# Kernel optimization log

Hardware: AMD Instinct MI355X
Metric: run time of the kernel (lower is better)

The kernel has to match this reference:

```python
import jax, jax.numpy as jnp
import numpy as np

B, S, D, U, L, DEG = 32, 256, 256, 256, 16, 16
N = B * S
E = N * DEG


def _xavier(k, shape, fan_in, fan_out):
    return jax.random.normal(k, shape, jnp.float32) * np.float32(np.sqrt(2.0 / (fan_in + fan_out)))


def setup_inputs() -> dict:
    key = jax.random.key(0)
    ks = jax.random.split(key, 16)
    src = jax.random.normal(ks[0], (S, B, D), jnp.float32)
    V_in = _xavier(ks[1], (L, D, U), D, U)
    b_in = jnp.zeros((L, U), jnp.float32)
    V_in_gate = _xavier(ks[2], (D, 1), D, 1)
    b_in_gate = jnp.ones((L, 1), jnp.float32)
    V_out = _xavier(ks[3], (L, D, U), D, U)
    b_out = jnp.zeros((L, U), jnp.float32)
    V_out_gate = _xavier(ks[4], (D, 1), D, 1)
    b_out_gate = jnp.ones((L, 1), jnp.float32)
    W_self_loop = _xavier(ks[5], (D, U), D, U)
    W_self_loop_gate = _xavier(ks[6], (D, 1), D, 1)
    arc_tensor_in = jnp.stack([jax.random.randint(ks[7], (E,), 0, B),
                               jax.random.randint(ks[8], (E,), 0, S)]).astype(jnp.int64)
    arc_tensor_out = jnp.stack([jax.random.randint(ks[9], (E,), 0, B),
                                jax.random.randint(ks[10], (E,), 0, S)]).astype(jnp.int64)
    label_tensor_in = jax.random.randint(ks[11], (1, E), 0, L).astype(jnp.int64)
    label_tensor_out = jax.random.randint(ks[12], (1, E), 0, L).astype(jnp.int64)
    mask_in = jnp.ones((N, DEG), jnp.float32)
    mask_out = jnp.ones((N, DEG), jnp.float32)
    mask_loop = jnp.ones((N, 1), jnp.float32)
    sent_mask = jnp.ones((S, B), jnp.float32)
    return {"src": src, "V_in": V_in, "b_in": b_in, "V_in_gate": V_in_gate,
            "b_in_gate": b_in_gate, "V_out": V_out, "b_out": b_out,
            "V_out_gate": V_out_gate, "b_out_gate": b_out_gate,
            "W_self_loop": W_self_loop, "W_self_loop_gate": W_self_loop_gate,
            "arc_tensor_in": arc_tensor_in, "arc_tensor_out": arc_tensor_out,
            "label_tensor_in": label_tensor_in, "label_tensor_out": label_tensor_out,
            "mask_in": mask_in, "mask_out": mask_out, "mask_loop": mask_loop,
            "sent_mask": sent_mask}


def _gcn_forward(src, V_in, b_in, V_in_gate, b_in_gate, V_out, b_out, V_out_gate,
                 b_out_gate, W_self_loop, W_self_loop_gate, mask_in, mask_out,
                 mask_loop, sent_mask, arc_tensor_in, arc_tensor_out,
                 label_tensor_in, label_tensor_out):
    S_, B_, D_ = src.shape
    U_ = V_in.shape[-1]
    enc = jnp.transpose(src, (1, 0, 2))            # [B,S,D]
    x = enc.reshape(B_ * S_, D_)                   # [N,D]

    def arc_branch(V, b, Vg, bg, arc, lab):
        # per-label transform of all nodes, as in the original: [L,N,U]
        all_lab = jnp.einsum('nd,ldu->lnu', x, V)
        idx = arc[0] * S_ + arc[1]                 # [E] flat node indices
        l = lab[0]                                  # [E] edge labels
        feats = all_lab[l, idx] + b[l]              # [E,U]
        deg = idx.shape[0] // (B_ * S_)
        feats = feats.reshape(B_, S_, deg, U_)
        g = (x @ Vg)[idx, 0] + bg[l, 0]             # [E]
        gate = g.reshape(B_, S_, deg)
        return feats, gate

    in_, in_gate = arc_branch(V_in, b_in, V_in_gate, b_in_gate, arc_tensor_in, label_tensor_in)
    out_, out_gate = arc_branch(V_out, b_out, V_out_gate, b_out_gate, arc_tensor_out, label_tensor_out)
    same = (x @ W_self_loop).reshape(B_, S_, 1, U_)
    same_gate = (x @ W_self_loop_gate).reshape(B_, S_, 1)

    pot = jnp.concatenate([in_, out_, same], axis=2)            # [B,S,maxdeg,U]
    pot_gate = jnp.concatenate([in_gate, out_gate, same_gate], axis=2)
    mask_soft = jnp.concatenate([mask_in, mask_out, mask_loop], axis=1)  # [N,maxdeg]
    md = pot.shape[2]
    pot = pot.reshape(B_ * S_, md, U_)
    probs = jax.nn.sigmoid(pot_gate.reshape(B_ * S_, md)) * mask_soft
    res = jax.nn.relu(jnp.sum(pot * probs[:, :, None], axis=1)).reshape(B_, S_, U_)
    res = res * sent_mask.T[:, :, None]
    return jnp.transpose(res, (1, 0, 2))            # [S,B,U]


def reference(src, V_in, b_in, V_in_gate, b_in_gate, V_out, b_out, V_out_gate,
              b_out_gate, W_self_loop, W_self_loop_gate, arc_tensor_in,
              arc_tensor_out, label_tensor_in, label_tensor_out, mask_in,
              mask_out, mask_loop, sent_mask):
    return _gcn_forward(src, V_in, b_in, V_in_gate, b_in_gate, V_out, b_out,
                        V_out_gate, b_out_gate, W_self_loop, W_self_loop_gate,
                        mask_in, mask_out, mask_loop, sent_mask,
                        arc_tensor_in, arc_tensor_out, label_tensor_in,
                        label_tensor_out)
```

## Files before the change

### kernel.cpp

```cpp
#include <hip/hip_runtime.h>
#include <hip/hip_bf16.h>

#define BB 32
#define SS 256
#define DD 256
#define UU 256
#define LL 16
#define DEG 16
#define NN (BB * SS)
#define EE (NN * DEG)
#define NSLICE 33
#define NSL2 34
#define KMAIN (NSLICE * DD)
#define KTOT (NSL2 * DD)
#define KSPLIT 8
#define KS (KTOT / KSPLIT)
#define TM 128
#define TN 256

using short8 = __attribute__((ext_vector_type(8))) short;
using f32x4  = __attribute__((ext_vector_type(4))) float;

#define GLDS(g, l)                                                        \
  __builtin_amdgcn_global_load_lds(                                       \
      (const __attribute__((address_space(1))) void*)(g),                 \
      (__attribute__((address_space(3))) void*)(l), 16, 0, 0)

__device__ __forceinline__ float bf2f(unsigned short v) {
  union { unsigned u; float f; } t;
  t.u = ((unsigned)v) << 16;
  return t.f;
}
__device__ __forceinline__ unsigned short f2bf(float f) {
  __hip_bfloat16 h = __float2bfloat16(f);
  return *(unsigned short*)&h;
}
__device__ __forceinline__ float sigm(float x) {
  return 1.f / (1.f + __expf(-x));
}

__global__ __launch_bounds__(256) void k_pre(
    const float* __restrict__ src, const float* __restrict__ gin,
    const float* __restrict__ gout, const float* __restrict__ gloop,
    const float* __restrict__ Vin, const float* __restrict__ Vout,
    const float* __restrict__ Wself, const float* __restrict__ b_in,
    const float* __restrict__ b_out,
    __hip_bfloat16* __restrict__ x_bf, float* __restrict__ xg_in,
    float* __restrict__ xg_out, float* __restrict__ xg_loop,
    __hip_bfloat16* __restrict__ Vt) {
  int bid = blockIdx.x;
  if (bid < NN) {
    int n = bid;
    int b = n / SS, s = n % SS;
    int d = threadIdx.x;
    float v = src[(size_t)(s * BB + b) * DD + d];
    x_bf[(size_t)n * DD + d] = __float2bfloat16(v);
    float p0 = v * gin[d], p1 = v * gout[d], p2 = v * gloop[d];
#pragma unroll
    for (int o = 32; o > 0; o >>= 1) {
      p0 += __shfl_down(p0, o);
      p1 += __shfl_down(p1, o);
      p2 += __shfl_down(p2, o);
    }
    __shared__ float r0[4], r1[4], r2[4];
    int w = threadIdx.x >> 6, lane = threadIdx.x & 63;
    if (lane == 0) { r0[w] = p0; r1[w] = p1; r2[w] = p2; }
    __syncthreads();
    if (threadIdx.x == 0) {
      xg_in[n]   = r0[0] + r0[1] + r0[2] + r0[3];
      xg_out[n]  = r1[0] + r1[1] + r1[2] + r1[3];
      xg_loop[n] = r2[0] + r2[1] + r2[2] + r2[3];
    }
    return;
  }
  int t = bid - NN;
  int z = t >> 6;
  int rem = t & 63;
  int bx = rem & 7, by = rem >> 3;
  int tid = threadIdx.x;
  int tx = tid & 31, ty = tid >> 5;
  if (z == NSLICE) {
    int u0 = bx * 32, j0 = by * 32;
#pragma unroll
    for (int i = 0; i < 4; i++) {
      int u = u0 + ty + i * 8, j = j0 + tx;
      float v = 0.f;
      if (j >= 1 && j <= LL)         v = b_in[(j - 1) * UU + u];
      else if (j > LL && j < NSLICE) v = b_out[(j - 1 - LL) * UU + u];
      Vt[(size_t)u * KTOT + KMAIN + j] = __float2bfloat16(v);
    }
    return;
  }
  __shared__ float tbuf[32][33];
  const float* srcM = (z == 0) ? Wself
                    : (z <= LL ? Vin  + (size_t)(z - 1)      * DD * UU
                               : Vout + (size_t)(z - 1 - LL) * DD * UU);
  int u0 = bx * 32, d0 = by * 32;
#pragma unroll
  for (int i = 0; i < 4; i++) {
    int dr = ty + i * 8;
    tbuf[dr][tx] = srcM[(size_t)(d0 + dr) * UU + u0 + tx];
  }
  __syncthreads();
#pragma unroll
  for (int i = 0; i < 4; i++) {
    int ur = ty + i * 8;
    Vt[(size_t)(u0 + ur) * KTOT + z * DD + d0 + tx] = __float2bfloat16(tbuf[tx][ur]);
  }
}

__global__ __launch_bounds__(256) void k_agg(
    const __hip_bfloat16* __restrict__ x,
    const float* __restrict__ xg_in, const float* __restrict__ xg_out,
    const float* __restrict__ xg_loop,
    const float* __restrict__ b_ing, const float* __restrict__ b_outg,
    const int* __restrict__ arc_in, const int* __restrict__ arc_out,
    const int* __restrict__ lab_in, const int* __restrict__ lab_out,
    const float* __restrict__ mask_in, const float* __restrict__ mask_out,
    const float* __restrict__ mask_loop,
    __hip_bfloat16* __restrict__ Y) {
  __shared__ int u_sl[4][32], u_src[4][32];
  __shared__ float u_w[4][32];
  __shared__ int s_sl[4][32], s_src[4][32];
  __shared__ float s_w[4][32];
  __shared__ float s_wsum[4][NSLICE];
  int wv = threadIdx.x >> 6, lane = threadIdx.x & 63;
  int n = blockIdx.x * 4 + wv;
  if (lane < 32) {
    int br = lane >> 4, k = lane & 15;
    int e = n * DEG + k;
    const int* a = br ? arc_out : arc_in;
    int l = (br ? lab_out : lab_in)[e];
    int srcn = a[e] * SS + a[EE + e];
    float g = (br ? xg_out : xg_in)[srcn] + (br ? b_outg : b_ing)[l];
    u_sl[wv][lane] = 1 + br * LL + l;
    u_src[wv][lane] = srcn;
    u_w[wv][lane] = sigm(g) * (br ? mask_out : mask_in)[e];
  }
  __syncthreads();
  if (lane < 32) {
    int my = u_sl[wv][lane];
    int rank = 0;
#pragma unroll
    for (int j = 0; j < 32; j++) {
      int oj = u_sl[wv][j];
      rank += (oj < my || (oj == my && j < lane)) ? 1 : 0;
    }
    s_sl[wv][rank] = my;
    s_src[wv][rank] = u_src[wv][lane];
    s_w[wv][rank] = u_w[wv][lane];
  }
  __syncthreads();

  const unsigned short* xp = (const unsigned short*)x;
  unsigned short* yp = (unsigned short*)Y;
  int d4 = lane * 4;
  {
    float wl = sigm(xg_loop[n]) * mask_loop[n];
    ushort4 v = *(const ushort4*)&xp[(size_t)n * DD + d4];
    ushort4 o;
    o.x = f2bf(wl * bf2f(v.x)); o.y = f2bf(wl * bf2f(v.y));
    o.z = f2bf(wl * bf2f(v.z)); o.w = f2bf(wl * bf2f(v.w));
    *(ushort4*)&yp[(size_t)n * DD + d4] = o;
  }
  unsigned long long present = 0ull;
  float a0 = 0.f, a1 = 0.f, a2 = 0.f, a3 = 0.f, ws = 0.f;
#pragma unroll
  for (int e = 0; e < 32; e++) {
    int sl = s_sl[wv][e];
    int srcn = s_src[wv][e];
    float w = s_w[wv][e];
    ushort4 v = *(const ushort4*)&xp[(size_t)srcn * DD + d4];
    a0 += w * bf2f(v.x); a1 += w * bf2f(v.y);
    a2 += w * bf2f(v.z); a3 += w * bf2f(v.w);
    ws += w;
    int slnext = (e < 31) ? s_sl[wv][e + 1] : 999;
    if (sl != slnext) {
      ushort4 o;
      o.x = f2bf(a0); o.y = f2bf(a1); o.z = f2bf(a2); o.w = f2bf(a3);
      *(ushort4*)&yp[((size_t)sl * NN + n) * DD + d4] = o;
      if (lane == 0) s_wsum[wv][sl] = ws;
      present |= (1ull << sl);
      a0 = a1 = a2 = a3 = ws = 0.f;
    }
  }
  ushort4 zero4 = {0, 0, 0, 0};
#pragma unroll
  for (int s = 1; s < NSLICE; s++) {
    if (!((present >> s) & 1ull)) {
      *(ushort4*)&yp[((size_t)s * NN + n) * DD + d4] = zero4;
      if (lane == 0) s_wsum[wv][s] = 0.f;
    }
  }
  __syncthreads();
  {
    ushort4 o;
    unsigned short* op = (unsigned short*)&o;
#pragma unroll
    for (int c = 0; c < 4; c++) {
      int j = d4 + c;
      float v = (j >= 1 && j < NSLICE) ? s_wsum[wv][j] : 0.f;
      op[c] = f2bf(v);
    }
    *(ushort4*)&yp[((size_t)NSLICE * NN + n) * DD + d4] = o;
  }
}

__global__ __launch_bounds__(256, 2) void k_gemm(
    const __hip_bfloat16* __restrict__ A, const __hip_bfloat16* __restrict__ Bt,
    __hip_bfloat16* __restrict__ partial) {
  __shared__ __align__(16) __hip_bfloat16 As[2][TM * 32];
  __shared__ __align__(16) __hip_bfloat16 Bs[2][TN * 32];
  __hip_bfloat16* P = partial + (size_t)blockIdx.y * NN * UU;
  int kbeg = blockIdx.y * KS;
  int row0 = blockIdx.x * TM;
  int tid = threadIdx.x;
  int w = tid >> 6, lane = tid & 63;
  int lrow = lane & 15, quad = lane >> 4;
  int sr = lane >> 2;
  int sc = (lane & 3) * 8;

#define STAGE(bufi, it)                                                     \
  {                                                                         \
    int k0 = kbeg + (it) * 32;                                              \
    int sl = k0 >> 8, dc = k0 & 255;                                        \
    const __hip_bfloat16* Ab = A + ((size_t)sl * NN + row0) * DD + dc;      \
    _Pragma("unroll")                                                       \
    for (int t = 0; t < 2; t++) {                                           \
      int rb = (w * 2 + t) * 16;                                            \
      GLDS(&Ab[(size_t)(rb + sr) * DD + sc], &As[bufi][rb * 32]);           \
    }                                                                       \
    _Pragma("unroll")                                                       \
    for (int t = 0; t < 4; t++) {                                           \
      int rb = (w * 4 + t) * 16;                                            \
      GLDS(&Bt[(size_t)(rb + sr) * KTOT + k0 + sc], &Bs[bufi][rb * 32]);    \
    }                                                                       \
  }

  STAGE(0, 0);
  f32x4 acc[8][4] = {};
  constexpr int NIT = KS / 32;
  for (int it = 0; it < NIT; it++) {
    int cur = it & 1;
    __syncthreads();
    if (it + 1 < NIT) STAGE(cur ^ 1, it + 1);
    short8 af[8], bfr[4];
#pragma unroll
    for (int i = 0; i < 8; i++)
      af[i] = *(const short8*)&As[cur][(i * 16 + lrow) * 32 + quad * 8];
#pragma unroll
    for (int j = 0; j < 4; j++)
      bfr[j] = *(const short8*)&Bs[cur][(w * 64 + j * 16 + lrow) * 32 + quad * 8];
#pragma unroll
    for (int j = 0; j < 4; j++)
#pragma unroll
      for (int i = 0; i < 8; i++)
        acc[i][j] = __builtin_amdgcn_mfma_f32_16x16x32_bf16(af[i], bfr[j], acc[i][j], 0, 0, 0);
  }
#undef STAGE
#pragma unroll
  for (int i = 0; i < 8; i++)
#pragma unroll
    for (int j = 0; j < 4; j++) {
      int col = w * 64 + j * 16 + lrow;
      int rowb = row0 + i * 16 + quad * 4;
#pragma unroll
      for (int r = 0; r < 4; r++)
        P[(size_t)(rowb + r) * UU + col] = __float2bfloat16(acc[i][j][r]);
    }
}

__global__ __launch_bounds__(256) void k_finish(
    const __hip_bfloat16* __restrict__ partial, const float* __restrict__ sent,
    float* __restrict__ out) {
  int wv = threadIdx.x >> 6, lane = threadIdx.x & 63;
  int n = blockIdx.x * 4 + wv;
  int u4 = lane * 4;
  size_t idx = (size_t)n * UU + u4;
  const unsigned short* pp = (const unsigned short*)partial;
  float a0 = 0.f, a1 = 0.f, a2 = 0.f, a3 = 0.f;
#pragma unroll
  for (int z = 0; z < KSPLIT; z++) {
    ushort4 v = *(const ushort4*)&pp[(size_t)z * NN * UU + idx];
    a0 += bf2f(v.x); a1 += bf2f(v.y); a2 += bf2f(v.z); a3 += bf2f(v.w);
  }
  int s = n % SS, b = n / SS;
  float sm = sent[s * BB + b];
  float4 o;
  o.x = fmaxf(a0, 0.f) * sm; o.y = fmaxf(a1, 0.f) * sm;
  o.z = fmaxf(a2, 0.f) * sm; o.w = fmaxf(a3, 0.f) * sm;
  *(float4*)&out[((size_t)s * BB + b) * UU + u4] = o;
}

extern "C" void kernel_launch(void* const* d_in, const int* in_sizes, int n_in,
                              void* d_out, int out_size, void* d_ws, size_t ws_size,
                              hipStream_t stream) {
  const float* src      = (const float*)d_in[0];
  const float* V_in     = (const float*)d_in[1];
  const float* b_in     = (const float*)d_in[2];
  const float* V_ing    = (const float*)d_in[3];
  const float* b_ing    = (const float*)d_in[4];
  const float* V_out    = (const float*)d_in[5];
  const float* b_out    = (const float*)d_in[6];
  const float* V_outg   = (const float*)d_in[7];
  const float* b_outg   = (const float*)d_in[8];
  const float* W_self   = (const float*)d_in[9];
  const float* W_selfg  = (const float*)d_in[10];
  const int* arc_in     = (const int*)d_in[11];
  const int* arc_out    = (const int*)d_in[12];
  const int* lab_in     = (const int*)d_in[13];
  const int* lab_out    = (const int*)d_in[14];
  const float* mask_in  = (const float*)d_in[15];
  const float* mask_out = (const float*)d_in[16];
  const float* mask_loop= (const float*)d_in[17];
  const float* sent     = (const float*)d_in[18];
  float* out = (float*)d_out;

  char* ws = (char*)d_ws;
  size_t off = 0;
  auto alloc = [&](size_t bytes) -> void* {
    void* p = ws + off;
    off += (bytes + 255) & ~(size_t)255;
    return p;
  };
  __hip_bfloat16* x_bf = (__hip_bfloat16*)alloc((size_t)NN * DD * 2);
  __hip_bfloat16* Vt   = (__hip_bfloat16*)alloc((size_t)UU * KTOT * 2);
  float* xg_in   = (float*)alloc(NN * 4);
  float* xg_out  = (float*)alloc(NN * 4);
  float* xg_loop = (float*)alloc(NN * 4);
  __hip_bfloat16* Y = (__hip_bfloat16*)alloc((size_t)NSL2 * NN * DD * 2);
  __hip_bfloat16* partial =
      (__hip_bfloat16*)alloc((size_t)KSPLIT * NN * UU * 2);

  k_pre<<<NN + (NSLICE + 1) * 64, 256, 0, stream>>>(
      src, V_ing, V_outg, W_selfg, V_in, V_out, W_self, b_in, b_out,
      x_bf, xg_in, xg_out, xg_loop, Vt);
  k_agg<<<NN / 4, 256, 0, stream>>>(x_bf, xg_in, xg_out, xg_loop, b_ing, b_outg,
                                    arc_in, arc_out, lab_in, lab_out,
                                    mask_in, mask_out, mask_loop, Y);
  k_gemm<<<dim3(NN / TM, KSPLIT), 256, 0, stream>>>(Y, Vt, partial);
  k_finish<<<NN / 4, 256, 0, stream>>>(partial, sent, out);
}
```

Before: 194.4 us.

## Fuse preprocessing into aggregation and swizzle GEMM LDS layout

```diff
diff --git a/kernel.cpp b/kernel.cpp
--- a/kernel.cpp
+++ b/kernel.cpp
@@ -17,6 +17,8 @@
 #define KS (KTOT / KSPLIT)
 #define TM 128
 #define TN 256
+#define NAGG (NN / 4)
+#define NWT ((NSLICE + 1) * 64)
 
 using short8 = __attribute__((ext_vector_type(8))) short;
 using f32x4  = __attribute__((ext_vector_type(4))) float;
@@ -39,41 +41,120 @@
   return 1.f / (1.f + __expf(-x));
 }
 
-__global__ __launch_bounds__(256) void k_pre(
+__global__ __launch_bounds__(256) void k_front(
     const float* __restrict__ src, const float* __restrict__ gin,
     const float* __restrict__ gout, const float* __restrict__ gloop,
     const float* __restrict__ Vin, const float* __restrict__ Vout,
     const float* __restrict__ Wself, const float* __restrict__ b_in,
-    const float* __restrict__ b_out,
-    __hip_bfloat16* __restrict__ x_bf, float* __restrict__ xg_in,
-    float* __restrict__ xg_out, float* __restrict__ xg_loop,
-    __hip_bfloat16* __restrict__ Vt) {
+    const float* __restrict__ b_out, const float* __restrict__ b_ing,
+    const float* __restrict__ b_outg,
+    const int* __restrict__ arc_in, const int* __restrict__ arc_out,
+    const int* __restrict__ lab_in, const int* __restrict__ lab_out,
+    const float* __restrict__ mask_in, const float* __restrict__ mask_out,
+    const float* __restrict__ mask_loop,
+    __hip_bfloat16* __restrict__ Vt, __hip_bfloat16* __restrict__ Y) {
+  __shared__ int u_sl[4][32], u_src[4][32];
+  __shared__ float u_bg[4][32], u_mask[4][32];
+  __shared__ int s_sl[4][32], s_src[4][32];
+  __shared__ float s_bg[4][32], s_mask[4][32];
+  __shared__ float s_wsum[4][NSLICE];
+  __shared__ float tbuf[32][33];
   int bid = blockIdx.x;
-  if (bid < NN) {
-    int n = bid;
-    int b = n / SS, s = n % SS;
-    int d = threadIdx.x;
-    float v = src[(size_t)(s * BB + b) * DD + d];
-    x_bf[(size_t)n * DD + d] = __float2bfloat16(v);
-    float p0 = v * gin[d], p1 = v * gout[d], p2 = v * gloop[d];
-#pragma unroll
-    for (int o = 32; o > 0; o >>= 1) {
-      p0 += __shfl_down(p0, o);
-      p1 += __shfl_down(p1, o);
-      p2 += __shfl_down(p2, o);
-    }
-    __shared__ float r0[4], r1[4], r2[4];
-    int w = threadIdx.x >> 6, lane = threadIdx.x & 63;
-    if (lane == 0) { r0[w] = p0; r1[w] = p1; r2[w] = p2; }
+  if (bid < NAGG) {
+    int wv = threadIdx.x >> 6, lane = threadIdx.x & 63;
+    int n = bid * 4 + wv;
+    if (lane < 32) {
+      int br = lane >> 4, k = lane & 15;
+      int e = n * DEG + k;
+      const int* a = br ? arc_out : arc_in;
+      int l = (br ? lab_out : lab_in)[e];
+      int srcn = a[e] * SS + a[EE + e];
+      u_sl[wv][lane] = 1 + br * LL + l;
+      u_src[wv][lane] = srcn;
+      u_bg[wv][lane] = (br ? b_outg : b_ing)[l];
+      u_mask[wv][lane] = (br ? mask_out : mask_in)[e];
+    }
     __syncthreads();
-    if (threadIdx.x == 0) {
-      xg_in[n]   = r0[0] + r0[1] + r0[2] + r0[3];
-      xg_out[n]  = r1[0] + r1[1] + r1[2] + r1[3];
-      xg_loop[n] = r2[0] + r2[1] + r2[2] + r2[3];
+    if (lane < 32) {
+      int my = u_sl[wv][lane];
+      int rank = 0;
+#pragma unroll
+      for (int j = 0; j < 32; j++) {
+        int oj = u_sl[wv][j];
+        rank += (oj < my || (oj == my && j < lane)) ? 1 : 0;
+      }
+      s_sl[wv][rank] = my;
+      s_src[wv][rank] = u_src[wv][lane];
+      s_bg[wv][rank] = u_bg[wv][lane];
+      s_mask[wv][rank] = u_mask[wv][lane];
+    }
+    __syncthreads();
+
+    unsigned short* yp = (unsigned short*)Y;
+    int d4 = lane * 4;
+    float4 gv_in  = *(const float4*)&gin[d4];
+    float4 gv_out = *(const float4*)&gout[d4];
+    {
+      const float* rp = src + (size_t)((n & 255) * BB + (n >> 8)) * DD;
+      float4 v = *(const float4*)&rp[d4];
+      float4 gl = *(const float4*)&gloop[d4];
+      float p = v.x * gl.x + v.y * gl.y + v.z * gl.z + v.w * gl.w;
+#pragma unroll
+      for (int o = 1; o < 64; o <<= 1) p += __shfl_xor(p, o);
+      float wl = sigm(p) * mask_loop[n];
+      ushort4 o4;
+      o4.x = f2bf(wl * v.x); o4.y = f2bf(wl * v.y);
+      o4.z = f2bf(wl * v.z); o4.w = f2bf(wl * v.w);
+      *(ushort4*)&yp[(size_t)n * DD + d4] = o4;
+    }
+    unsigned long long present = 0ull;
+    float a0 = 0.f, a1 = 0.f, a2 = 0.f, a3 = 0.f, ws = 0.f;
+#pragma unroll
+    for (int e = 0; e < 32; e++) {
+      int sl = s_sl[wv][e];
+      int srcn = s_src[wv][e];
+      const float* rp = src + (size_t)((srcn & 255) * BB + (srcn >> 8)) * DD;
+      float4 v = *(const float4*)&rp[d4];
+      float4 gv = (sl <= LL) ? gv_in : gv_out;
+      float p = v.x * gv.x + v.y * gv.y + v.z * gv.z + v.w * gv.w;
+#pragma unroll
+      for (int o = 1; o < 64; o <<= 1) p += __shfl_xor(p, o);
+      float w = sigm(p + s_bg[wv][e]) * s_mask[wv][e];
+      a0 += w * v.x; a1 += w * v.y; a2 += w * v.z; a3 += w * v.w;
+      ws += w;
+      int slnext = (e < 31) ? s_sl[wv][e + 1] : 999;
+      if (sl != slnext) {
+        ushort4 o4;
+        o4.x = f2bf(a0); o4.y = f2bf(a1); o4.z = f2bf(a2); o4.w = f2bf(a3);
+        *(ushort4*)&yp[((size_t)sl * NN + n) * DD + d4] = o4;
+        if (lane == 0) s_wsum[wv][sl] = ws;
+        present |= (1ull << sl);
+        a0 = a1 = a2 = a3 = ws = 0.f;
+      }
+    }
+    ushort4 zero4 = {0, 0, 0, 0};
+#pragma unroll
+    for (int s = 1; s < NSLICE; s++) {
+      if (!((present >> s) & 1ull)) {
+        *(ushort4*)&yp[((size_t)s * NN + n) * DD + d4] = zero4;
+        if (lane == 0) s_wsum[wv][s] = 0.f;
+      }
+    }
+    __syncthreads();
+    {
+      ushort4 o4;
+      unsigned short* op = (unsigned short*)&o4;
+#pragma unroll
+      for (int c = 0; c < 4; c++) {
+        int j = d4 + c;
+        float v = (j >= 1 && j < NSLICE) ? s_wsum[wv][j] : 0.f;
+        op[c] = f2bf(v);
+      }
+      *(ushort4*)&yp[((size_t)NSLICE * NN + n) * DD + d4] = o4;
     }
     return;
   }
-  int t = bid - NN;
+  int t = bid - NAGG;
   int z = t >> 6;
   int rem = t & 63;
   int bx = rem & 7, by = rem >> 3;
@@ -91,7 +172,6 @@
     }
     return;
   }
-  __shared__ float tbuf[32][33];
   const float* srcM = (z == 0) ? Wself
                     : (z <= LL ? Vin  + (size_t)(z - 1)      * DD * UU
                                : Vout + (size_t)(z - 1 - LL) * DD * UU);
@@ -106,103 +186,6 @@
   for (int i = 0; i < 4; i++) {
     int ur = ty + i * 8;
     Vt[(size_t)(u0 + ur) * KTOT + z * DD + d0 + tx] = __float2bfloat16(tbuf[tx][ur]);
-  }
-}
-
-__global__ __launch_bounds__(256) void k_agg(
-    const __hip_bfloat16* __restrict__ x,
-    const float* __restrict__ xg_in, const float* __restrict__ xg_out,
-    const float* __restrict__ xg_loop,
-    const float* __restrict__ b_ing, const float* __restrict__ b_outg,
-    const int* __restrict__ arc_in, const int* __restrict__ arc_out,
-    const int* __restrict__ lab_in, const int* __restrict__ lab_out,
-    const float* __restrict__ mask_in, const float* __restrict__ mask_out,
-    const float* __restrict__ mask_loop,
-    __hip_bfloat16* __restrict__ Y) {
-  __shared__ int u_sl[4][32], u_src[4][32];
-  __shared__ float u_w[4][32];
-  __shared__ int s_sl[4][32], s_src[4][32];
-  __shared__ float s_w[4][32];
-  __shared__ float s_wsum[4][NSLICE];
-  int wv = threadIdx.x >> 6, lane = threadIdx.x & 63;
-  int n = blockIdx.x * 4 + wv;
-  if (lane < 32) {
-    int br = lane >> 4, k = lane & 15;
-    int e = n * DEG + k;
-    const int* a = br ? arc_out : arc_in;
-    int l = (br ? lab_out : lab_in)[e];
-    int srcn = a[e] * SS + a[EE + e];
-    float g = (br ? xg_out : xg_in)[srcn] + (br ? b_outg : b_ing)[l];
-    u_sl[wv][lane] = 1 + br * LL + l;
-    u_src[wv][lane] = srcn;
-    u_w[wv][lane] = sigm(g) * (br ? mask_out : mask_in)[e];
-  }
-  __syncthreads();
-  if (lane < 32) {
-    int my = u_sl[wv][lane];
-    int rank = 0;
-#pragma unroll
-    for (int j = 0; j < 32; j++) {
-      int oj = u_sl[wv][j];
-      rank += (oj < my || (oj == my && j < lane)) ? 1 : 0;
-    }
-    s_sl[wv][rank] = my;
-    s_src[wv][rank] = u_src[wv][lane];
-    s_w[wv][rank] = u_w[wv][lane];
-  }
-  __syncthreads();
-
-  const unsigned short* xp = (const unsigned short*)x;
-  unsigned short* yp = (unsigned short*)Y;
-  int d4 = lane * 4;
-  {
-    float wl = sigm(xg_loop[n]) * mask_loop[n];
-    ushort4 v = *(const ushort4*)&xp[(size_t)n * DD + d4];
-    ushort4 o;
-    o.x = f2bf(wl * bf2f(v.x)); o.y = f2bf(wl * bf2f(v.y));
-    o.z = f2bf(wl * bf2f(v.z)); o.w = f2bf(wl * bf2f(v.w));
-    *(ushort4*)&yp[(size_t)n * DD + d4] = o;
-  }
-  unsigned long long present = 0ull;
-  float a0 = 0.f, a1 = 0.f, a2 = 0.f, a3 = 0.f, ws = 0.f;
-#pragma unroll
-  for (int e = 0; e < 32; e++) {
-    int sl = s_sl[wv][e];
-    int srcn = s_src[wv][e];
-    float w = s_w[wv][e];
-    ushort4 v = *(const ushort4*)&xp[(size_t)srcn * DD + d4];
-    a0 += w * bf2f(v.x); a1 += w * bf2f(v.y);
-    a2 += w * bf2f(v.z); a3 += w * bf2f(v.w);
-    ws += w;
-    int slnext = (e < 31) ? s_sl[wv][e + 1] : 999;
-    if (sl != slnext) {
-      ushort4 o;
-      o.x = f2bf(a0); o.y = f2bf(a1); o.z = f2bf(a2); o.w = f2bf(a3);
-      *(ushort4*)&yp[((size_t)sl * NN + n) * DD + d4] = o;
-      if (lane == 0) s_wsum[wv][sl] = ws;
-      present |= (1ull << sl);
-      a0 = a1 = a2 = a3 = ws = 0.f;
-    }
-  }
-  ushort4 zero4 = {0, 0, 0, 0};
-#pragma unroll
-  for (int s = 1; s < NSLICE; s++) {
-    if (!((present >> s) & 1ull)) {
-      *(ushort4*)&yp[((size_t)s * NN + n) * DD + d4] = zero4;
-      if (lane == 0) s_wsum[wv][s] = 0.f;
-    }
-  }
-  __syncthreads();
-  {
-    ushort4 o;
-    unsigned short* op = (unsigned short*)&o;
-#pragma unroll
-    for (int c = 0; c < 4; c++) {
-      int j = d4 + c;
-      float v = (j >= 1 && j < NSLICE) ? s_wsum[wv][j] : 0.f;
-      op[c] = f2bf(v);
-    }
-    *(ushort4*)&yp[((size_t)NSLICE * NN + n) * DD + d4] = o;
   }
 }
 
@@ -218,7 +201,8 @@
   int w = tid >> 6, lane = tid & 63;
   int lrow = lane & 15, quad = lane >> 4;
   int sr = lane >> 2;
-  int sc = (lane & 3) * 8;
+  int swz = (((lane & 3) ^ (sr & 3)) * 8);
+  int rchunk = (quad ^ (lrow & 3)) * 8;
 
 #define STAGE(bufi, it)                                                     \
   {                                                                         \
@@ -228,12 +212,12 @@
     _Pragma("unroll")                                                       \
     for (int t = 0; t < 2; t++) {                                           \
       int rb = (w * 2 + t) * 16;                                            \
-      GLDS(&Ab[(size_t)(rb + sr) * DD + sc], &As[bufi][rb * 32]);           \
+      GLDS(&Ab[(size_t)(rb + sr) * DD + swz], &As[bufi][rb * 32]);          \
     }                                                                       \
     _Pragma("unroll")                                                       \
     for (int t = 0; t < 4; t++) {                                           \
       int rb = (w * 4 + t) * 16;                                            \
-      GLDS(&Bt[(size_t)(rb + sr) * KTOT + k0 + sc], &Bs[bufi][rb * 32]);    \
+      GLDS(&Bt[(size_t)(rb + sr) * KTOT + k0 + swz], &Bs[bufi][rb * 32]);   \
     }                                                                       \
   }
 
@@ -247,10 +231,10 @@
     short8 af[8], bfr[4];
 #pragma unroll
     for (int i = 0; i < 8; i++)
-      af[i] = *(const short8*)&As[cur][(i * 16 + lrow) * 32 + quad * 8];
+      af[i] = *(const short8*)&As[cur][(i * 16 + lrow) * 32 + rchunk];
 #pragma unroll
     for (int j = 0; j < 4; j++)
-      bfr[j] = *(const short8*)&Bs[cur][(w * 64 + j * 16 + lrow) * 32 + quad * 8];
+      bfr[j] = *(const short8*)&Bs[cur][(w * 64 + j * 16 + lrow) * 32 + rchunk];
 #pragma unroll
     for (int j = 0; j < 4; j++)
 #pragma unroll
@@ -323,21 +307,15 @@
     off += (bytes + 255) & ~(size_t)255;
     return p;
   };
-  __hip_bfloat16* x_bf = (__hip_bfloat16*)alloc((size_t)NN * DD * 2);
-  __hip_bfloat16* Vt   = (__hip_bfloat16*)alloc((size_t)UU * KTOT * 2);
-  float* xg_in   = (float*)alloc(NN * 4);
-  float* xg_out  = (float*)alloc(NN * 4);
-  float* xg_loop = (float*)alloc(NN * 4);
-  __hip_bfloat16* Y = (__hip_bfloat16*)alloc((size_t)NSL2 * NN * DD * 2);
+  __hip_bfloat16* Vt = (__hip_bfloat16*)alloc((size_t)UU * KTOT * 2);
+  __hip_bfloat16* Y  = (__hip_bfloat16*)alloc((size_t)NSL2 * NN * DD * 2);
   __hip_bfloat16* partial =
       (__hip_bfloat16*)alloc((size_t)KSPLIT * NN * UU * 2);
 
-  k_pre<<<NN + (NSLICE + 1) * 64, 256, 0, stream>>>(
+  k_front<<<NAGG + NWT, 256, 0, stream>>>(
       src, V_ing, V_outg, W_selfg, V_in, V_out, W_self, b_in, b_out,
-      x_bf, xg_in, xg_out, xg_loop, Vt);
-  k_agg<<<NN / 4, 256, 0, stream>>>(x_bf, xg_in, xg_out, xg_loop, b_ing, b_outg,
-                                    arc_in, arc_out, lab_in, lab_out,
-                                    mask_in, mask_out, mask_loop, Y);
+      b_ing, b_outg, arc_in, arc_out, lab_in, lab_out,
+      mask_in, mask_out, mask_loop, Vt, Y);
   k_gemm<<<dim3(NN / TM, KSPLIT), 256, 0, stream>>>(Y, Vt, partial);
   k_finish<<<NN / 4, 256, 0, stream>>>(partial, sent, out);
 }
```

Measured after the change: 206.0 us. 6.0% more time.
